# Performance work log

Hardware: AMD Instinct MI355X
Metric: run time of the kernel (lower is better)

Reference implementation:

```python
import jax, jax.numpy as jnp
import numpy as np

N, D, E, G, L = 65536, 512, 1048576, 128, 512


def setup_inputs() -> dict:
    key = jax.random.key(0)
    ks = jax.random.split(key, 12)
    s = 0.02
    # disjoint sequence groups: a permutation of all nodes reshaped to [G, L]
    seq_ids = jax.random.permutation(ks[0], N).reshape(G, L)
    return {
        'in_feats': jax.random.normal(ks[1], (N, D), jnp.float32),
        'edge_src': jax.random.randint(ks[2], (E,), 0, N),
        'edge_dst': jax.random.randint(ks[3], (E,), 0, N),
        'seq_ids': seq_ids,
        'W_conv': jax.random.normal(ks[4], (D, D), jnp.float32) * s,
        'b_conv': jnp.zeros((D,), jnp.float32),
        'W_ff1': jax.random.normal(ks[5], (D, D), jnp.float32) * s,
        'b_ff1': jnp.zeros((D,), jnp.float32),
        'W_ih': jax.random.normal(ks[6], (3 * D, D), jnp.float32) * s,
        'W_hh': jax.random.normal(ks[7], (3 * D, D), jnp.float32) * s,
        'b_ih': jnp.zeros((3 * D,), jnp.float32),
        'b_hh': jnp.zeros((3 * D,), jnp.float32),
        'W_ff2': jax.random.normal(ks[8], (D, D), jnp.float32) * s,
        'b_ff2': jnp.zeros((D,), jnp.float32),
    }


def _gru(x_lgd, W_ih, W_hh, b_ih, b_hh):
    # x_lgd: [L, G, D] (seq-major, batch_first=False); torch nn.GRU cell math
    d = W_hh.shape[1]
    # precompute input gates for all steps: [L, G, 3D]
    gi_all = jnp.einsum('lgd,ed->lge', x_lgd, W_ih) + b_ih

    def step(h, gi):
        gh = h @ W_hh.T + b_hh
        ir, iz, inn = jnp.split(gi, 3, axis=-1)
        hr, hz, hn = jnp.split(gh, 3, axis=-1)
        r = jax.nn.sigmoid(ir + hr)
        z = jax.nn.sigmoid(iz + hz)
        n = jnp.tanh(inn + r * hn)
        h_new = (1.0 - z) * n + z * h
        return h_new, h_new

    h0 = jnp.zeros((x_lgd.shape[1], d), x_lgd.dtype)
    _, ys = jax.lax.scan(step, h0, gi_all)
    return ys  # [L, G, D]


def reference(in_feats, edge_src, edge_dst, seq_ids, W_conv, b_conv,
              W_ff1, b_ff1, W_ih, W_hh, b_ih, b_hh, W_ff2, b_ff2):
    # conv_layer: mean aggregation over incoming edges, then Linear
    agg = jax.ops.segment_sum(in_feats[edge_src], edge_dst, num_segments=N)
    deg = jax.ops.segment_sum(jnp.ones((E,), in_feats.dtype), edge_dst, num_segments=N)
    agg = agg / jnp.maximum(deg, 1.0)[:, None]
    med = agg @ W_conv + b_conv                      # [N, D]
    # ff1
    med = jax.nn.relu(med @ W_ff1 + b_ff1)           # [N, D]
    # per-group seq_layer: gather [G, L, D], run GRU over L, scatter back
    seqs = med[seq_ids]                              # [G, L, D]
    ys = _gru(jnp.swapaxes(seqs, 0, 1), W_ih, W_hh, b_ih, b_hh)  # [L, G, D]
    ys = jnp.swapaxes(ys, 0, 1)                      # [G, L, D]
    # output[ids] += temp - output[ids]  ==  output[ids] = temp (disjoint ids)
    output = med.at[seq_ids.reshape(-1)].set(ys.reshape(-1, med.shape[-1]))
    # ff2
    return output @ W_ff2 + b_ff2
```

## Files before the change

kernel.cpp:

```cpp
#include <hip/hip_runtime.h>
#include <hip/hip_bf16.h>
#include <stdint.h>

typedef __hip_bfloat16 bf16;
typedef __attribute__((ext_vector_type(8))) short short8;
typedef __attribute__((ext_vector_type(4))) float f32x4;
typedef __attribute__((ext_vector_type(4))) unsigned int u32x4;
typedef __attribute__((ext_vector_type(2))) unsigned int u32x2;

#define NN 65536
#define DD 512
#define EE 1048576
#define GG 128
#define LL 512

static __device__ __forceinline__ void gld_lds16(const void* g, void* l) {
  __builtin_amdgcn_global_load_lds((const __attribute__((address_space(1))) uint32_t*)g,
                                   (__attribute__((address_space(3))) uint32_t*)l, 16, 0, 0);
}

__global__ __launch_bounds__(256) void k_prep(
    const float* __restrict__ Wc, const float* __restrict__ Wf1, const float* __restrict__ Wf2,
    const float* __restrict__ Wih, const float* __restrict__ Whh,
    bf16* __restrict__ WcT, bf16* __restrict__ Wf1T, bf16* __restrict__ Wf2T,
    bf16* __restrict__ WihB, bf16* __restrict__ WhhB)
{
  const int i = blockIdx.x * 256 + threadIdx.x;
  if (i < 512 * 512) {
    const int k = i >> 9, n = i & 511;
    WcT [n * 512 + k] = __float2bfloat16(Wc [i]);
    Wf1T[n * 512 + k] = __float2bfloat16(Wf1[i]);
    Wf2T[n * 512 + k] = __float2bfloat16(Wf2[i]);
  }
  if (i < 1536 * 512) {
    WihB[i] = __float2bfloat16(Wih[i]);
    WhhB[i] = __float2bfloat16(Whh[i]);
  }
}

__global__ __launch_bounds__(256) void k_cast(const float* __restrict__ f, bf16* __restrict__ o) {
  const long i = (long)(blockIdx.x * 256 + threadIdx.x) * 4;
  const float4 v = *(const float4*)&f[i];
  union { bf16 b[4]; ushort4 u; } pk;
  pk.b[0] = __float2bfloat16(v.x);
  pk.b[1] = __float2bfloat16(v.y);
  pk.b[2] = __float2bfloat16(v.z);
  pk.b[3] = __float2bfloat16(v.w);
  *(ushort4*)&o[i] = pk.u;
}

__global__ __launch_bounds__(256) void k_deg(const int* __restrict__ dst, int* __restrict__ deg) {
  const int e = blockIdx.x * 256 + threadIdx.x;
  atomicAdd(&deg[dst[e]], 1);
}

__global__ __launch_bounds__(1024) void k_scan1(const int* __restrict__ deg,
                                                int* __restrict__ roff, int* __restrict__ partial) {
  __shared__ int sd[1024];
  const int t = threadIdx.x, b = blockIdx.x, i = b * 1024 + t;
  const int v = deg[i];
  sd[t] = v;
  __syncthreads();
  for (int off = 1; off < 1024; off <<= 1) {
    int add = (t >= off) ? sd[t - off] : 0;
    __syncthreads();
    sd[t] += add;
    __syncthreads();
  }
  roff[i] = sd[t] - v;
  if (t == 1023) partial[b] = sd[t];
}

__global__ __launch_bounds__(64) void k_scan2(const int* __restrict__ partial, int* __restrict__ base) {
  __shared__ int sd[64];
  const int t = threadIdx.x;
  const int v = partial[t];
  sd[t] = v;
  __syncthreads();
  for (int off = 1; off < 64; off <<= 1) {
    int add = (t >= off) ? sd[t - off] : 0;
    __syncthreads();
    sd[t] += add;
    __syncthreads();
  }
  base[t] = sd[t] - v;
  if (t == 63) base[64] = sd[63];
}

__global__ __launch_bounds__(1024) void k_scan3(const int* __restrict__ base,
                                                int* __restrict__ roff, int* __restrict__ cursor) {
  const int b = blockIdx.x, t = threadIdx.x, i = b * 1024 + t;
  const int v = roff[i] + base[b];
  roff[i] = v;
  cursor[i] = v;
  if (i == 0) roff[NN] = base[64];
}

__global__ __launch_bounds__(256) void k_fill(const int* __restrict__ src, const int* __restrict__ dst,
                                              int* __restrict__ cursor, int* __restrict__ csr) {
  const int e = blockIdx.x * 256 + threadIdx.x;
  const int p = atomicAdd(&cursor[dst[e]], 1);
  csr[p] = src[e];
}

__global__ __launch_bounds__(128) void k_agg(
    const bf16* __restrict__ featsb, const int* __restrict__ csr,
    const int* __restrict__ roff, bf16* __restrict__ agg)
{
  const int n = blockIdx.x, t = threadIdx.x;
  const int s0 = roff[n], s1 = roff[n + 1];
  float a0 = 0.f, a1 = 0.f, a2 = 0.f, a3 = 0.f;
  for (int i = s0; i < s1; ++i) {
    const int s = csr[i];
    const ushort4 v = *(const ushort4*)&featsb[(long)s * 512 + t * 4];
    bf16 b0, b1, b2, b3;
    *(uint16_t*)&b0 = v.x; *(uint16_t*)&b1 = v.y;
    *(uint16_t*)&b2 = v.z; *(uint16_t*)&b3 = v.w;
    a0 += __bfloat162float(b0); a1 += __bfloat162float(b1);
    a2 += __bfloat162float(b2); a3 += __bfloat162float(b3);
  }
  const float sc = 1.f / fmaxf((float)(s1 - s0), 1.f);
  union { bf16 b[4]; ushort4 u; } pk;
  pk.b[0] = __float2bfloat16(a0 * sc);
  pk.b[1] = __float2bfloat16(a1 * sc);
  pk.b[2] = __float2bfloat16(a2 * sc);
  pk.b[3] = __float2bfloat16(a3 * sc);
  *(ushort4*)&agg[(long)n * 512 + t * 4] = pk.u;
}

template<bool GATHER, bool RELU>
__global__ __launch_bounds__(256) void k_gemm(
    const bf16* __restrict__ A, const bf16* __restrict__ Bt,
    const float* __restrict__ bias, const int* __restrict__ gidx,
    bf16* __restrict__ outb, int Ncols)
{
  __shared__ bf16 lsA[128 * 64];
  __shared__ bf16 lsB[128 * 64];
  const int t = threadIdx.x;
  const int lane = t & 63, wid = t >> 6;
  const int wr = wid >> 1, wc = wid & 1;
  const int tm = blockIdx.y * 128, tn = blockIdx.x * 128;
  const int col8 = (t & 7) * 8;
  const int rsub = t >> 3;
  const int lc = lane & 15, lk = lane >> 4;

  long arow[4], brow[4];
#pragma unroll
  for (int i = 0; i < 4; ++i) {
    const int r = tm + i * 32 + rsub;
    int ar = r;
    if constexpr (GATHER) ar = gidx[r];
    arow[i] = (long)ar * 512;
    brow[i] = (long)(tn + i * 32 + rsub) * 512;
  }

  f32x4 acc[4][4];
#pragma unroll
  for (int a = 0; a < 4; ++a)
#pragma unroll
    for (int b = 0; b < 4; ++b) acc[a][b] = (f32x4){0.f, 0.f, 0.f, 0.f};

  for (int ks = 0; ks < 8; ++ks) {
    const int k0 = ks * 64;
#pragma unroll
    for (int i = 0; i < 4; ++i) {
      gld_lds16(A  + arow[i] + k0 + col8, &lsA[i * 2048 + t * 8]);
      gld_lds16(Bt + brow[i] + k0 + col8, &lsB[i * 2048 + t * 8]);
    }
    __syncthreads();
#pragma unroll
    for (int kk = 0; kk < 2; ++kk) {
      short8 af[4], bfr[4];
#pragma unroll
      for (int mi = 0; mi < 4; ++mi)
        af[mi] = *(const short8*)&lsA[(wr * 64 + mi * 16 + lc) * 64 + kk * 32 + lk * 8];
#pragma unroll
      for (int ni = 0; ni < 4; ++ni)
        bfr[ni] = *(const short8*)&lsB[(wc * 64 + ni * 16 + lc) * 64 + kk * 32 + lk * 8];
#pragma unroll
      for (int mi = 0; mi < 4; ++mi)
#pragma unroll
        for (int ni = 0; ni < 4; ++ni)
          acc[mi][ni] = __builtin_amdgcn_mfma_f32_16x16x32_bf16(af[mi], bfr[ni], acc[mi][ni], 0, 0, 0);
    }
    __syncthreads();
  }

  float bv[4];
#pragma unroll
  for (int ni = 0; ni < 4; ++ni) bv[ni] = bias[tn + wc * 64 + ni * 16 + lc];

#pragma unroll
  for (int mi = 0; mi < 4; ++mi) {
    const int r0 = tm + wr * 64 + mi * 16 + lk * 4;
#pragma unroll
    for (int j = 0; j < 4; ++j) {
      const int row = r0 + j;
      const long orow = (long)row * Ncols;
#pragma unroll
      for (int ni = 0; ni < 4; ++ni) {
        float v = acc[mi][ni][j] + bv[ni];
        if constexpr (RELU) v = fmaxf(v, 0.f);
        const int c = tn + wc * 64 + ni * 16 + lc;
        outb[orow + c] = __float2bfloat16(v);
      }
    }
  }
}

__global__ __launch_bounds__(256) void k_gemm_ys(
    const uint8_t* __restrict__ Ay, const bf16* __restrict__ Bt,
    const float* __restrict__ bias, const int* __restrict__ gidx,
    float* __restrict__ outf)
{
  __shared__ bf16 lsA[128 * 64];
  __shared__ bf16 lsB[128 * 64];
  const int t = threadIdx.x;
  const int lane = t & 63, wid = t >> 6;
  const int wr = wid >> 1, wc = wid & 1;
  const int tm = blockIdx.y * 128, tn = blockIdx.x * 128;
  const int col8 = (t & 7) * 8;
  const int rsub = t >> 3;
  const int lc = lane & 15, lk = lane >> 4;

  long arow[4], brow[4];
#pragma unroll
  for (int i = 0; i < 4; ++i) {
    const int r = tm + i * 32 + rsub;
    const int g = r >> 9, l = r & 511;
    arow[i] = ((long)l * 8 + (g >> 4)) * 16384 + (g & 15) * 32;
    brow[i] = (long)(tn + i * 32 + rsub) * 512;
  }

  f32x4 acc[4][4];
#pragma unroll
  for (int a = 0; a < 4; ++a)
#pragma unroll
    for (int b = 0; b < 4; ++b) acc[a][b] = (f32x4){0.f, 0.f, 0.f, 0.f};

  for (int ks = 0; ks < 8; ++ks) {
    const int k0 = ks * 64;
    const int kk16 = k0 + col8;
    const long aoff = ((long)(kk16 >> 4) << 9) + ((kk16 & 15) << 1);
#pragma unroll
    for (int i = 0; i < 4; ++i) {
      gld_lds16(Ay + arow[i] + aoff, &lsA[i * 2048 + t * 8]);
      gld_lds16(Bt + brow[i] + k0 + col8, &lsB[i * 2048 + t * 8]);
    }
    __syncthreads();
#pragma unroll
    for (int kk = 0; kk < 2; ++kk) {
      short8 af[4], bfr[4];
#pragma unroll
      for (int mi = 0; mi < 4; ++mi)
        af[mi] = *(const short8*)&lsA[(wr * 64 + mi * 16 + lc) * 64 + kk * 32 + lk * 8];
#pragma unroll
      for (int ni = 0; ni < 4; ++ni)
        bfr[ni] = *(const short8*)&lsB[(wc * 64 + ni * 16 + lc) * 64 + kk * 32 + lk * 8];
#pragma unroll
      for (int mi = 0; mi < 4; ++mi)
#pragma unroll
        for (int ni = 0; ni < 4; ++ni)
          acc[mi][ni] = __builtin_amdgcn_mfma_f32_16x16x32_bf16(af[mi], bfr[ni], acc[mi][ni], 0, 0, 0);
    }
    __syncthreads();
  }

  float bv[4];
#pragma unroll
  for (int ni = 0; ni < 4; ++ni) bv[ni] = bias[tn + wc * 64 + ni * 16 + lc];

#pragma unroll
  for (int mi = 0; mi < 4; ++mi) {
    const int r0 = tm + wr * 64 + mi * 16 + lk * 4;
#pragma unroll
    for (int j = 0; j < 4; ++j) {
      const int row = r0 + j;
      const long orow = (long)gidx[row] * 512;
#pragma unroll
      for (int ni = 0; ni < 4; ++ni) {
        const int c = tn + wc * 64 + ni * 16 + lc;
        outf[orow + c] = acc[mi][ni][j] + bv[ni];
      }
    }
  }
}

__global__ __launch_bounds__(128, 1) void k_gru12(
    const bf16* __restrict__ Whh, const float* __restrict__ bhh,
    const bf16* __restrict__ gi, uint8_t* __restrict__ ys2, int* __restrict__ flags)
{
  __shared__ bf16 lsW[96 * 520];
  const int t = threadIdx.x, lane = t & 63, w = t >> 6;
  const int chain = blockIdx.x >> 4, jcb = blockIdx.x & 15;
  const int lc = lane & 15, lk = lane >> 4;
  const int g0 = chain * 16;
  const int cols0 = jcb * 32;
  const int p = jcb * 2 + w;
  const int d0 = p * 16 + lk * 4;

#pragma unroll
  for (int it = 0; it < 48; ++it) {
    const int c = it * 128 + t;
    const int row = c >> 6, col8 = (c & 63) * 8;
    const int e = ((row >> 5) << 9) + cols0 + (row & 31);
    *(uint4*)&lsW[row * 520 + col8] = *(const uint4*)&Whh[(long)e * 512 + col8];
  }
  __syncthreads();

  float bRa[4], bZa[4], bNa[4];
#pragma unroll
  for (int j = 0; j < 4; ++j) {
    bRa[j] = bhh[d0 + j];
    bZa[j] = bhh[512 + d0 + j];
    bNa[j] = bhh[1024 + d0 + j];
  }
  float hreg[4] = {0.f, 0.f, 0.f, 0.f};

  const bf16* gp = gi + (long)(g0 + lc) * 786432 + d0;
  uint8_t* psto = ys2 + (long)chain * 16384 + p * 512 + lc * 32 + lk * 8;
  const long laneoff = (long)(lk >> 1) * 512 + lc * 32 + (lk & 1) * 16;

  int* chflags = flags + chain * 32 * 32;
  int* myflag  = chflags + p * 32;

  for (int l = 0; l < 512; ++l) {
    u32x2 gRv, gZv, gNv;
    asm volatile("global_load_dwordx2 %0, %1, off"             : "=v"(gRv) : "v"(gp) : "memory");
    asm volatile("global_load_dwordx2 %0, %1, off offset:1024" : "=v"(gZv) : "v"(gp) : "memory");
    asm volatile("global_load_dwordx2 %0, %1, off offset:2048" : "=v"(gNv) : "v"(gp) : "memory");
    gp += 1536;

    f32x4 acc[3] = { (f32x4){0.f,0.f,0.f,0.f}, (f32x4){0.f,0.f,0.f,0.f}, (f32x4){0.f,0.f,0.f,0.f} };
    if (l > 0) {
      int ok;
      do {
        const int v = __hip_atomic_load(&chflags[(lane & 31) * 32], __ATOMIC_RELAXED,
                                        __HIP_MEMORY_SCOPE_AGENT);
        ok = __all(v >= l);
      } while (!ok);
      asm volatile("" ::: "memory");

      const uint8_t* pb = ys2 + ((long)(l - 1) * 8 + chain) * 16384 + laneoff;
      u32x4 hv[16];
#pragma unroll
      for (int q = 0; q < 4; ++q) {
        const uint8_t* pbq = pb + q * 4096;
#pragma unroll
        for (int r2 = 0; r2 < 4; ++r2)
          asm volatile("global_load_dwordx4 %0, %1, off offset:%2 sc0 sc1"
                       : "=v"(hv[q * 4 + r2]) : "v"(pbq), "n"(r2 * 1024) : "memory");
      }
      asm volatile("s_waitcnt vmcnt(0)" ::: "memory");
      __builtin_amdgcn_sched_barrier(0);

#pragma unroll
      for (int kk = 0; kk < 16; ++kk) {
        union { u32x4 u; short8 s; } cv;
        cv.u = hv[kk];
#pragma unroll
        for (int gate = 0; gate < 3; ++gate) {
          const short8 wfr = *(const short8*)&lsW[(gate * 32 + w * 16 + lc) * 520 + kk * 32 + lk * 8];
          acc[gate] = __builtin_amdgcn_mfma_f32_16x16x32_bf16(wfr, cv.s, acc[gate], 0, 0, 0);
        }
      }
    } else {
      asm volatile("s_waitcnt vmcnt(0)" ::: "memory");
      __builtin_amdgcn_sched_barrier(0);
    }

    uint32_t hb[4];
#pragma unroll
    for (int j = 0; j < 4; ++j) {
      const uint32_t sh = (j & 1) * 16;
      union { uint32_t u; float f; } cR, cZ, cN;
      cR.u = ((gRv[j >> 1] >> sh) & 0xffffu) << 16;
      cZ.u = ((gZv[j >> 1] >> sh) & 0xffffu) << 16;
      cN.u = ((gNv[j >> 1] >> sh) & 0xffffu) << 16;
      const float r = 1.f / (1.f + __expf(-(cR.f + acc[0][j] + bRa[j])));
      const float z = 1.f / (1.f + __expf(-(cZ.f + acc[1][j] + bZa[j])));
      const float x2 = cN.f + r * (acc[2][j] + bNa[j]);
      const float ex = __expf(2.f * x2);
      const float n = 1.f - 2.f / (ex + 1.f);
      const float hn = (1.f - z) * n + z * hreg[j];
      hreg[j] = hn;
      const bf16 hnb = __float2bfloat16(hn);
      hb[j] = (uint32_t)(*(const uint16_t*)&hnb);
    }
    u32x2 hp;
    hp[0] = hb[0] | (hb[1] << 16);
    hp[1] = hb[2] | (hb[3] << 16);
    asm volatile("global_store_dwordx2 %0, %1, off sc0 sc1" :: "v"(psto), "v"(hp) : "memory");
    psto += 131072;
    asm volatile("s_waitcnt vmcnt(0)" ::: "memory");
    if (lane == 0)
      __hip_atomic_store(myflag, l + 1, __ATOMIC_RELAXED, __HIP_MEMORY_SCOPE_AGENT);
  }
}

extern "C" void kernel_launch(void* const* d_in, const int* in_sizes, int n_in,
                              void* d_out, int out_size, void* d_ws, size_t ws_size,
                              hipStream_t stream)
{
  (void)in_sizes; (void)n_in; (void)out_size; (void)ws_size;
  const float* in_feats = (const float*)d_in[0];
  const int*   e_src    = (const int*)d_in[1];
  const int*   e_dst    = (const int*)d_in[2];
  const int*   seq      = (const int*)d_in[3];
  const float* W_conv   = (const float*)d_in[4];
  const float* b_conv   = (const float*)d_in[5];
  const float* W_ff1    = (const float*)d_in[6];
  const float* b_ff1    = (const float*)d_in[7];
  const float* W_ih     = (const float*)d_in[8];
  const float* W_hh     = (const float*)d_in[9];
  const float* b_ih     = (const float*)d_in[10];
  const float* b_hh     = (const float*)d_in[11];
  const float* W_ff2    = (const float*)d_in[12];
  const float* b_ff2    = (const float*)d_in[13];

  uint8_t* ws = (uint8_t*)d_ws;
  int*  deg     = (int*) (ws + 0);
  int*  cursor  = (int*) (ws + 262144u);
  int*  roff    = (int*) (ws + 524288u);
  bf16* WcT     = (bf16*)(ws + 1048576u);
  bf16* Wf1T    = (bf16*)(ws + 1572864u);
  bf16* Wf2T    = (bf16*)(ws + 2097152u);
  bf16* WihB    = (bf16*)(ws + 2621440u);
  bf16* WhhB    = (bf16*)(ws + 4194304u);
  int*  csr     = (int*) (ws + 6291456u);
  int*  flags   = (int*) (ws + 10485760u);
  int*  partial = (int*) (ws + 10616832u);
  int*  sbase   = (int*) (ws + 10620928u);
  bf16* med2    = (bf16*)(ws + 16777216u);
  uint8_t* ys2  = (uint8_t*)med2;
  bf16* gib     = (bf16*)(ws + 83886080u);
  bf16* aggb    = (bf16*)(ws + 83886080u);
  bf16* med1    = (bf16*)(ws + 150994944u);
  bf16* featsb  = (bf16*)(ws + 150994944u);

  hipMemsetAsync(deg,   0, NN * 4,          stream);
  hipMemsetAsync(flags, 0, 8 * 32 * 32 * 4, stream);

  k_prep <<<3072, 256, 0, stream>>>(W_conv, W_ff1, W_ff2, W_ih, W_hh, WcT, Wf1T, Wf2T, WihB, WhhB);
  k_cast <<<NN * DD / 1024, 256, 0, stream>>>(in_feats, featsb);
  k_deg  <<<EE / 256, 256, 0, stream>>>(e_dst, deg);
  k_scan1<<<64, 1024, 0, stream>>>(deg, roff, partial);
  k_scan2<<<1, 64, 0, stream>>>(partial, sbase);
  k_scan3<<<64, 1024, 0, stream>>>(sbase, roff, cursor);
  k_fill <<<EE / 256, 256, 0, stream>>>(e_src, e_dst, cursor, csr);
  k_agg  <<<NN, 128, 0, stream>>>(featsb, csr, roff, aggb);

  dim3 g512(4, 512), g1536(12, 512);
  k_gemm<false, false><<<g512,  256, 0, stream>>>(aggb, WcT,  b_conv, nullptr, med1, 512);
  k_gemm<false, true ><<<g512,  256, 0, stream>>>(med1, Wf1T, b_ff1,  nullptr, med2, 512);
  k_gemm<true,  false><<<g1536, 256, 0, stream>>>(med2, WihB, b_ih,   seq,     gib,  1536);

  k_gru12<<<128, 128, 0, stream>>>(WhhB, b_hh, gib, ys2, flags);

  k_gemm_ys<<<g512, 256, 0, stream>>>(ys2, Wf2T, b_ff2, seq, (float*)d_out);
}
```

Baseline: 2.430 ms.

## Use one wave per GRU block covering 32 columns; unroll edge aggregation by four

The GRU recurrence kernel now runs one 64-thread wave per block, and each wave computes two 16-column tiles. This halves the number of producer flags that every step must poll, from 32 to 16 per chain, which shortens the cross-block barrier latency on the serial critical path. In exchange, each wave does twice the MFMA and gate work per step, and the weight loading into LDS is done by fewer threads. Separately, the aggregation gather loop is unrolled by four with bit-shift bf16-to-float conversion, so more feature loads are in flight at once.

```diff
diff --git a/kernel.cpp b/kernel.cpp
--- a/kernel.cpp
+++ b/kernel.cpp
@@ -110,14 +110,29 @@
   const int n = blockIdx.x, t = threadIdx.x;
   const int s0 = roff[n], s1 = roff[n + 1];
   float a0 = 0.f, a1 = 0.f, a2 = 0.f, a3 = 0.f;
-  for (int i = s0; i < s1; ++i) {
+  int i = s0;
+  for (; i + 4 <= s1; i += 4) {
+    const int sA = csr[i], sB = csr[i + 1], sC = csr[i + 2], sD = csr[i + 3];
+    const ushort4 vA = *(const ushort4*)&featsb[(long)sA * 512 + t * 4];
+    const ushort4 vB = *(const ushort4*)&featsb[(long)sB * 512 + t * 4];
+    const ushort4 vC = *(const ushort4*)&featsb[(long)sC * 512 + t * 4];
+    const ushort4 vD = *(const ushort4*)&featsb[(long)sD * 512 + t * 4];
+    union { uint32_t u; float f; } c;
+    c.u = (uint32_t)vA.x << 16; a0 += c.f;  c.u = (uint32_t)vA.y << 16; a1 += c.f;
+    c.u = (uint32_t)vA.z << 16; a2 += c.f;  c.u = (uint32_t)vA.w << 16; a3 += c.f;
+    c.u = (uint32_t)vB.x << 16; a0 += c.f;  c.u = (uint32_t)vB.y << 16; a1 += c.f;
+    c.u = (uint32_t)vB.z << 16; a2 += c.f;  c.u = (uint32_t)vB.w << 16; a3 += c.f;
+    c.u = (uint32_t)vC.x << 16; a0 += c.f;  c.u = (uint32_t)vC.y << 16; a1 += c.f;
+    c.u = (uint32_t)vC.z << 16; a2 += c.f;  c.u = (uint32_t)vC.w << 16; a3 += c.f;
+    c.u = (uint32_t)vD.x << 16; a0 += c.f;  c.u = (uint32_t)vD.y << 16; a1 += c.f;
+    c.u = (uint32_t)vD.z << 16; a2 += c.f;  c.u = (uint32_t)vD.w << 16; a3 += c.f;
+  }
+  for (; i < s1; ++i) {
     const int s = csr[i];
     const ushort4 v = *(const ushort4*)&featsb[(long)s * 512 + t * 4];
-    bf16 b0, b1, b2, b3;
-    *(uint16_t*)&b0 = v.x; *(uint16_t*)&b1 = v.y;
-    *(uint16_t*)&b2 = v.z; *(uint16_t*)&b3 = v.w;
-    a0 += __bfloat162float(b0); a1 += __bfloat162float(b1);
-    a2 += __bfloat162float(b2); a3 += __bfloat162float(b3);
+    union { uint32_t u; float f; } c;
+    c.u = (uint32_t)v.x << 16; a0 += c.f;  c.u = (uint32_t)v.y << 16; a1 += c.f;
+    c.u = (uint32_t)v.z << 16; a2 += c.f;  c.u = (uint32_t)v.w << 16; a3 += c.f;
   }
   const float sc = 1.f / fmaxf((float)(s1 - s0), 1.f);
   union { bf16 b[4]; ushort4 u; } pk;
@@ -286,56 +301,59 @@
   }
 }
 
-__global__ __launch_bounds__(128, 1) void k_gru12(
+__global__ __launch_bounds__(64, 1) void k_gru13(
     const bf16* __restrict__ Whh, const float* __restrict__ bhh,
     const bf16* __restrict__ gi, uint8_t* __restrict__ ys2, int* __restrict__ flags)
 {
   __shared__ bf16 lsW[96 * 520];
-  const int t = threadIdx.x, lane = t & 63, w = t >> 6;
-  const int chain = blockIdx.x >> 4, jcb = blockIdx.x & 15;
+  const int t = threadIdx.x, lane = t & 63;
+  const int chain = blockIdx.x >> 4, p = blockIdx.x & 15;
   const int lc = lane & 15, lk = lane >> 4;
   const int g0 = chain * 16;
-  const int cols0 = jcb * 32;
-  const int p = jcb * 2 + w;
-  const int d0 = p * 16 + lk * 4;
-
-#pragma unroll
-  for (int it = 0; it < 48; ++it) {
-    const int c = it * 128 + t;
+  const int cols0 = p * 32;
+  const int d0a = cols0 + lk * 4;
+  const int d0b = cols0 + 16 + lk * 4;
+
+  for (int it = 0; it < 96; ++it) {
+    const int c = it * 64 + t;
     const int row = c >> 6, col8 = (c & 63) * 8;
     const int e = ((row >> 5) << 9) + cols0 + (row & 31);
     *(uint4*)&lsW[row * 520 + col8] = *(const uint4*)&Whh[(long)e * 512 + col8];
   }
   __syncthreads();
 
-  float bRa[4], bZa[4], bNa[4];
+  float bRa[4], bZa[4], bNa[4], bRb[4], bZb[4], bNb[4];
 #pragma unroll
   for (int j = 0; j < 4; ++j) {
-    bRa[j] = bhh[d0 + j];
-    bZa[j] = bhh[512 + d0 + j];
-    bNa[j] = bhh[1024 + d0 + j];
-  }
-  float hreg[4] = {0.f, 0.f, 0.f, 0.f};
-
-  const bf16* gp = gi + (long)(g0 + lc) * 786432 + d0;
-  uint8_t* psto = ys2 + (long)chain * 16384 + p * 512 + lc * 32 + lk * 8;
+    bRa[j] = bhh[d0a + j];  bZa[j] = bhh[512 + d0a + j];  bNa[j] = bhh[1024 + d0a + j];
+    bRb[j] = bhh[d0b + j];  bZb[j] = bhh[512 + d0b + j];  bNb[j] = bhh[1024 + d0b + j];
+  }
+  float hregA[4] = {0.f, 0.f, 0.f, 0.f};
+  float hregB[4] = {0.f, 0.f, 0.f, 0.f};
+
+  const bf16* gp = gi + (long)(g0 + lc) * 786432 + d0a;
+  uint8_t* psto = ys2 + (long)chain * 16384 + p * 1024 + lc * 32 + lk * 8;
   const long laneoff = (long)(lk >> 1) * 512 + lc * 32 + (lk & 1) * 16;
 
-  int* chflags = flags + chain * 32 * 32;
+  int* chflags = flags + chain * 16 * 32;
   int* myflag  = chflags + p * 32;
 
   for (int l = 0; l < 512; ++l) {
-    u32x2 gRv, gZv, gNv;
-    asm volatile("global_load_dwordx2 %0, %1, off"             : "=v"(gRv) : "v"(gp) : "memory");
-    asm volatile("global_load_dwordx2 %0, %1, off offset:1024" : "=v"(gZv) : "v"(gp) : "memory");
-    asm volatile("global_load_dwordx2 %0, %1, off offset:2048" : "=v"(gNv) : "v"(gp) : "memory");
+    u32x2 gRa, gZa, gNa, gRb, gZb, gNb;
+    asm volatile("global_load_dwordx2 %0, %1, off"             : "=v"(gRa) : "v"(gp) : "memory");
+    asm volatile("global_load_dwordx2 %0, %1, off offset:1024" : "=v"(gZa) : "v"(gp) : "memory");
+    asm volatile("global_load_dwordx2 %0, %1, off offset:2048" : "=v"(gNa) : "v"(gp) : "memory");
+    asm volatile("global_load_dwordx2 %0, %1, off offset:32"   : "=v"(gRb) : "v"(gp) : "memory");
+    asm volatile("global_load_dwordx2 %0, %1, off offset:1056" : "=v"(gZb) : "v"(gp) : "memory");
+    asm volatile("global_load_dwordx2 %0, %1, off offset:2080" : "=v"(gNb) : "v"(gp) : "memory");
     gp += 1536;
 
-    f32x4 acc[3] = { (f32x4){0.f,0.f,0.f,0.f}, (f32x4){0.f,0.f,0.f,0.f}, (f32x4){0.f,0.f,0.f,0.f} };
+    f32x4 accA[3] = { (f32x4){0.f,0.f,0.f,0.f}, (f32x4){0.f,0.f,0.f,0.f}, (f32x4){0.f,0.f,0.f,0.f} };
+    f32x4 accB[3] = { (f32x4){0.f,0.f,0.f,0.f}, (f32x4){0.f,0.f,0.f,0.f}, (f32x4){0.f,0.f,0.f,0.f} };
     if (l > 0) {
       int ok;
       do {
-        const int v = __hip_atomic_load(&chflags[(lane & 31) * 32], __ATOMIC_RELAXED,
+        const int v = __hip_atomic_load(&chflags[(lane & 15) * 32], __ATOMIC_RELAXED,
                                         __HIP_MEMORY_SCOPE_AGENT);
         ok = __all(v >= l);
       } while (!ok);
@@ -360,8 +378,10 @@
         cv.u = hv[kk];
 #pragma unroll
         for (int gate = 0; gate < 3; ++gate) {
-          const short8 wfr = *(const short8*)&lsW[(gate * 32 + w * 16 + lc) * 520 + kk * 32 + lk * 8];
-          acc[gate] = __builtin_amdgcn_mfma_f32_16x16x32_bf16(wfr, cv.s, acc[gate], 0, 0, 0);
+          const short8 wfA = *(const short8*)&lsW[(gate * 32 + lc) * 520 + kk * 32 + lk * 8];
+          const short8 wfB = *(const short8*)&lsW[(gate * 32 + 16 + lc) * 520 + kk * 32 + lk * 8];
+          accA[gate] = __builtin_amdgcn_mfma_f32_16x16x32_bf16(wfA, cv.s, accA[gate], 0, 0, 0);
+          accB[gate] = __builtin_amdgcn_mfma_f32_16x16x32_bf16(wfB, cv.s, accB[gate], 0, 0, 0);
         }
       }
     } else {
@@ -369,28 +389,46 @@
       __builtin_amdgcn_sched_barrier(0);
     }
 
-    uint32_t hb[4];
+    uint32_t hbA[4], hbB[4];
 #pragma unroll
     for (int j = 0; j < 4; ++j) {
       const uint32_t sh = (j & 1) * 16;
       union { uint32_t u; float f; } cR, cZ, cN;
-      cR.u = ((gRv[j >> 1] >> sh) & 0xffffu) << 16;
-      cZ.u = ((gZv[j >> 1] >> sh) & 0xffffu) << 16;
-      cN.u = ((gNv[j >> 1] >> sh) & 0xffffu) << 16;
-      const float r = 1.f / (1.f + __expf(-(cR.f + acc[0][j] + bRa[j])));
-      const float z = 1.f / (1.f + __expf(-(cZ.f + acc[1][j] + bZa[j])));
-      const float x2 = cN.f + r * (acc[2][j] + bNa[j]);
+      cR.u = ((gRa[j >> 1] >> sh) & 0xffffu) << 16;
+      cZ.u = ((gZa[j >> 1] >> sh) & 0xffffu) << 16;
+      cN.u = ((gNa[j >> 1] >> sh) & 0xffffu) << 16;
+      const float r = 1.f / (1.f + __expf(-(cR.f + accA[0][j] + bRa[j])));
+      const float z = 1.f / (1.f + __expf(-(cZ.f + accA[1][j] + bZa[j])));
+      const float x2 = cN.f + r * (accA[2][j] + bNa[j]);
       const float ex = __expf(2.f * x2);
       const float n = 1.f - 2.f / (ex + 1.f);
-      const float hn = (1.f - z) * n + z * hreg[j];
-      hreg[j] = hn;
+      const float hn = (1.f - z) * n + z * hregA[j];
+      hregA[j] = hn;
       const bf16 hnb = __float2bfloat16(hn);
-      hb[j] = (uint32_t)(*(const uint16_t*)&hnb);
-    }
-    u32x2 hp;
-    hp[0] = hb[0] | (hb[1] << 16);
-    hp[1] = hb[2] | (hb[3] << 16);
-    asm volatile("global_store_dwordx2 %0, %1, off sc0 sc1" :: "v"(psto), "v"(hp) : "memory");
+      hbA[j] = (uint32_t)(*(const uint16_t*)&hnb);
+    }
+#pragma unroll
+    for (int j = 0; j < 4; ++j) {
+      const uint32_t sh = (j & 1) * 16;
+      union { uint32_t u; float f; } cR, cZ, cN;
+      cR.u = ((gRb[j >> 1] >> sh) & 0xffffu) << 16;
+      cZ.u = ((gZb[j >> 1] >> sh) & 0xffffu) << 16;
+      cN.u = ((gNb[j >> 1] >> sh) & 0xffffu) << 16;
+      const float r = 1.f / (1.f + __expf(-(cR.f + accB[0][j] + bRb[j])));
+      const float z = 1.f / (1.f + __expf(-(cZ.f + accB[1][j] + bZb[j])));
+      const float x2 = cN.f + r * (accB[2][j] + bNb[j]);
+      const float ex = __expf(2.f * x2);
+      const float n = 1.f - 2.f / (ex + 1.f);
+      const float hn = (1.f - z) * n + z * hregB[j];
+      hregB[j] = hn;
+      const bf16 hnb = __float2bfloat16(hn);
+      hbB[j] = (uint32_t)(*(const uint16_t*)&hnb);
+    }
+    u32x2 hpA, hpB;
+    hpA[0] = hbA[0] | (hbA[1] << 16);  hpA[1] = hbA[2] | (hbA[3] << 16);
+    hpB[0] = hbB[0] | (hbB[1] << 16);  hpB[1] = hbB[2] | (hbB[3] << 16);
+    asm volatile("global_store_dwordx2 %0, %1, off sc0 sc1" :: "v"(psto),       "v"(hpA) : "memory");
+    asm volatile("global_store_dwordx2 %0, %1, off offset:512 sc0 sc1" :: "v"(psto), "v"(hpB) : "memory");
     psto += 131072;
     asm volatile("s_waitcnt vmcnt(0)" ::: "memory");
     if (lane == 0)
@@ -439,7 +477,7 @@
   bf16* featsb  = (bf16*)(ws + 150994944u);
 
   hipMemsetAsync(deg,   0, NN * 4,          stream);
-  hipMemsetAsync(flags, 0, 8 * 32 * 32 * 4, stream);
+  hipMemsetAsync(flags, 0, 8 * 16 * 32 * 4, stream);
 
   k_prep <<<3072, 256, 0, stream>>>(W_conv, W_ff1, W_ff2, W_ih, W_hh, WcT, Wf1T, Wf2T, WihB, WhhB);
   k_cast <<<NN * DD / 1024, 256, 0, stream>>>(in_feats, featsb);
@@ -455,7 +493,7 @@
   k_gemm<false, true ><<<g512,  256, 0, stream>>>(med1, Wf1T, b_ff1,  nullptr, med2, 512);
   k_gemm<true,  false><<<g1536, 256, 0, stream>>>(med2, WihB, b_ih,   seq,     gib,  1536);
 
-  k_gru12<<<128, 128, 0, stream>>>(WhhB, b_hh, gib, ys2, flags);
+  k_gru13<<<128, 64, 0, stream>>>(WhhB, b_hh, gib, ys2, flags);
 
   k_gemm_ys<<<g512, 256, 0, stream>>>(ys2, Wf2T, b_ff2, seq, (float*)d_out);
 }
```

New measurement: 2.767 ms. 13.9% more time.

## Interleave two GRU chains per block and unroll neighbor aggregation by four

Applied to the files above, without the earlier changes.

The GRU recurrence kernel now launches 64 blocks, and each block processes two independent 16-sequence chains (A and B) in alternation. While one chain waits on its cross-block flag synchronization, the other's phase can proceed, with each chain's W_hh slice in LDS shared by both. Phases within a block still run sequentially, so the latency hiding depends on chain B's peers making progress while chain A waits. Separately, the edge aggregation loop is unrolled by four with independent gathers, and bf16 is widened to float with a plain shift.

```diff
diff --git a/kernel.cpp b/kernel.cpp
--- a/kernel.cpp
+++ b/kernel.cpp
@@ -110,14 +110,29 @@
   const int n = blockIdx.x, t = threadIdx.x;
   const int s0 = roff[n], s1 = roff[n + 1];
   float a0 = 0.f, a1 = 0.f, a2 = 0.f, a3 = 0.f;
-  for (int i = s0; i < s1; ++i) {
+  int i = s0;
+  for (; i + 4 <= s1; i += 4) {
+    const int sA = csr[i], sB = csr[i + 1], sC = csr[i + 2], sD = csr[i + 3];
+    const ushort4 vA = *(const ushort4*)&featsb[(long)sA * 512 + t * 4];
+    const ushort4 vB = *(const ushort4*)&featsb[(long)sB * 512 + t * 4];
+    const ushort4 vC = *(const ushort4*)&featsb[(long)sC * 512 + t * 4];
+    const ushort4 vD = *(const ushort4*)&featsb[(long)sD * 512 + t * 4];
+    union { uint32_t u; float f; } c;
+    c.u = (uint32_t)vA.x << 16; a0 += c.f;  c.u = (uint32_t)vA.y << 16; a1 += c.f;
+    c.u = (uint32_t)vA.z << 16; a2 += c.f;  c.u = (uint32_t)vA.w << 16; a3 += c.f;
+    c.u = (uint32_t)vB.x << 16; a0 += c.f;  c.u = (uint32_t)vB.y << 16; a1 += c.f;
+    c.u = (uint32_t)vB.z << 16; a2 += c.f;  c.u = (uint32_t)vB.w << 16; a3 += c.f;
+    c.u = (uint32_t)vC.x << 16; a0 += c.f;  c.u = (uint32_t)vC.y << 16; a1 += c.f;
+    c.u = (uint32_t)vC.z << 16; a2 += c.f;  c.u = (uint32_t)vC.w << 16; a3 += c.f;
+    c.u = (uint32_t)vD.x << 16; a0 += c.f;  c.u = (uint32_t)vD.y << 16; a1 += c.f;
+    c.u = (uint32_t)vD.z << 16; a2 += c.f;  c.u = (uint32_t)vD.w << 16; a3 += c.f;
+  }
+  for (; i < s1; ++i) {
     const int s = csr[i];
     const ushort4 v = *(const ushort4*)&featsb[(long)s * 512 + t * 4];
-    bf16 b0, b1, b2, b3;
-    *(uint16_t*)&b0 = v.x; *(uint16_t*)&b1 = v.y;
-    *(uint16_t*)&b2 = v.z; *(uint16_t*)&b3 = v.w;
-    a0 += __bfloat162float(b0); a1 += __bfloat162float(b1);
-    a2 += __bfloat162float(b2); a3 += __bfloat162float(b3);
+    union { uint32_t u; float f; } c;
+    c.u = (uint32_t)v.x << 16; a0 += c.f;  c.u = (uint32_t)v.y << 16; a1 += c.f;
+    c.u = (uint32_t)v.z << 16; a2 += c.f;  c.u = (uint32_t)v.w << 16; a3 += c.f;
   }
   const float sc = 1.f / fmaxf((float)(s1 - s0), 1.f);
   union { bf16 b[4]; ushort4 u; } pk;
@@ -286,15 +301,82 @@
   }
 }
 
-__global__ __launch_bounds__(128, 1) void k_gru12(
+#define GRU_PHASE(CCH, CF, MF, GR, GZ, GN, HREG, PST)                                       \
+  {                                                                                          \
+    f32x4 acc[3] = { (f32x4){0.f,0.f,0.f,0.f}, (f32x4){0.f,0.f,0.f,0.f},                     \
+                     (f32x4){0.f,0.f,0.f,0.f} };                                             \
+    if (l > 0) {                                                                             \
+      int ok;                                                                                \
+      do {                                                                                   \
+        const int v = __hip_atomic_load(&(CF)[(lane & 31) * 32], __ATOMIC_RELAXED,           \
+                                        __HIP_MEMORY_SCOPE_AGENT);                           \
+        ok = __all(v >= l);                                                                  \
+      } while (!ok);                                                                         \
+      asm volatile("" ::: "memory");                                                         \
+      const uint8_t* pb = ys2 + ((long)(l - 1) * 8 + (CCH)) * 16384 + laneoff;               \
+      u32x4 hv[16];                                                                          \
+      _Pragma("unroll")                                                                      \
+      for (int q = 0; q < 4; ++q) {                                                          \
+        const uint8_t* pbq = pb + q * 4096;                                                  \
+        _Pragma("unroll")                                                                    \
+        for (int r2 = 0; r2 < 4; ++r2)                                                       \
+          asm volatile("global_load_dwordx4 %0, %1, off offset:%2 sc0 sc1"                   \
+                       : "=v"(hv[q * 4 + r2]) : "v"(pbq), "n"(r2 * 1024) : "memory");        \
+      }                                                                                      \
+      asm volatile("s_waitcnt vmcnt(0)" ::: "memory");                                       \
+      __builtin_amdgcn_sched_barrier(0);                                                     \
+      _Pragma("unroll")                                                                      \
+      for (int kk = 0; kk < 16; ++kk) {                                                      \
+        union { u32x4 u; short8 s; } cv;                                                     \
+        cv.u = hv[kk];                                                                       \
+        _Pragma("unroll")                                                                    \
+        for (int gate = 0; gate < 3; ++gate) {                                               \
+          const short8 wfr = *(const short8*)&lsW[(gate * 32 + w * 16 + lc) * 520            \
+                                                  + kk * 32 + lk * 8];                       \
+          acc[gate] = __builtin_amdgcn_mfma_f32_16x16x32_bf16(wfr, cv.s, acc[gate], 0, 0, 0);\
+        }                                                                                    \
+      }                                                                                      \
+    } else {                                                                                 \
+      asm volatile("s_waitcnt vmcnt(0)" ::: "memory");                                       \
+      __builtin_amdgcn_sched_barrier(0);                                                     \
+    }                                                                                        \
+    uint32_t hb[4];                                                                          \
+    _Pragma("unroll")                                                                        \
+    for (int j = 0; j < 4; ++j) {                                                            \
+      const uint32_t sh = (j & 1) * 16;                                                      \
+      union { uint32_t u; float f; } cR, cZ, cN;                                             \
+      cR.u = (((GR)[j >> 1] >> sh) & 0xffffu) << 16;                                         \
+      cZ.u = (((GZ)[j >> 1] >> sh) & 0xffffu) << 16;                                         \
+      cN.u = (((GN)[j >> 1] >> sh) & 0xffffu) << 16;                                         \
+      const float r = 1.f / (1.f + __expf(-(cR.f + acc[0][j] + bRa[j])));                    \
+      const float z = 1.f / (1.f + __expf(-(cZ.f + acc[1][j] + bZa[j])));                    \
+      const float x2 = cN.f + r * (acc[2][j] + bNa[j]);                                      \
+      const float ex = __expf(2.f * x2);                                                     \
+      const float n = 1.f - 2.f / (ex + 1.f);                                                \
+      const float hn = (1.f - z) * n + z * (HREG)[j];                                        \
+      (HREG)[j] = hn;                                                                        \
+      const bf16 hnb = __float2bfloat16(hn);                                                 \
+      hb[j] = (uint32_t)(*(const uint16_t*)&hnb);                                            \
+    }                                                                                        \
+    u32x2 hp;                                                                                \
+    hp[0] = hb[0] | (hb[1] << 16);                                                           \
+    hp[1] = hb[2] | (hb[3] << 16);                                                           \
+    asm volatile("global_store_dwordx2 %0, %1, off sc0 sc1"                                  \
+                 :: "v"((PST) + (long)l * 131072), "v"(hp) : "memory");                      \
+    asm volatile("s_waitcnt vmcnt(0)" ::: "memory");                                         \
+    if (lane == 0)                                                                           \
+      __hip_atomic_store(MF, l + 1, __ATOMIC_RELAXED, __HIP_MEMORY_SCOPE_AGENT);             \
+  }
+
+__global__ __launch_bounds__(128, 1) void k_gru15(
     const bf16* __restrict__ Whh, const float* __restrict__ bhh,
     const bf16* __restrict__ gi, uint8_t* __restrict__ ys2, int* __restrict__ flags)
 {
   __shared__ bf16 lsW[96 * 520];
   const int t = threadIdx.x, lane = t & 63, w = t >> 6;
-  const int chain = blockIdx.x >> 4, jcb = blockIdx.x & 15;
+  const int jcb = blockIdx.x & 15, cpair = blockIdx.x >> 4;
+  const int cA = cpair, cB = cpair + 4;
   const int lc = lane & 15, lk = lane >> 4;
-  const int g0 = chain * 16;
   const int cols0 = jcb * 32;
   const int p = jcb * 2 + w;
   const int d0 = p * 16 + lk * 4;
@@ -315,88 +397,36 @@
     bZa[j] = bhh[512 + d0 + j];
     bNa[j] = bhh[1024 + d0 + j];
   }
-  float hreg[4] = {0.f, 0.f, 0.f, 0.f};
-
-  const bf16* gp = gi + (long)(g0 + lc) * 786432 + d0;
-  uint8_t* psto = ys2 + (long)chain * 16384 + p * 512 + lc * 32 + lk * 8;
+  float hregA[4] = {0.f, 0.f, 0.f, 0.f};
+  float hregB[4] = {0.f, 0.f, 0.f, 0.f};
+
+  const bf16* gpA = gi + (long)(cA * 16 + lc) * 786432 + d0;
+  const bf16* gpB = gi + (long)(cB * 16 + lc) * 786432 + d0;
+  uint8_t* psA = ys2 + (long)cA * 16384 + p * 512 + lc * 32 + lk * 8;
+  uint8_t* psB = ys2 + (long)cB * 16384 + p * 512 + lc * 32 + lk * 8;
   const long laneoff = (long)(lk >> 1) * 512 + lc * 32 + (lk & 1) * 16;
 
-  int* chflags = flags + chain * 32 * 32;
-  int* myflag  = chflags + p * 32;
+  int* cfA = flags + cA * 32 * 32;
+  int* cfB = flags + cB * 32 * 32;
+  int* mfA = cfA + p * 32;
+  int* mfB = cfB + p * 32;
 
   for (int l = 0; l < 512; ++l) {
-    u32x2 gRv, gZv, gNv;
-    asm volatile("global_load_dwordx2 %0, %1, off"             : "=v"(gRv) : "v"(gp) : "memory");
-    asm volatile("global_load_dwordx2 %0, %1, off offset:1024" : "=v"(gZv) : "v"(gp) : "memory");
-    asm volatile("global_load_dwordx2 %0, %1, off offset:2048" : "=v"(gNv) : "v"(gp) : "memory");
-    gp += 1536;
-
-    f32x4 acc[3] = { (f32x4){0.f,0.f,0.f,0.f}, (f32x4){0.f,0.f,0.f,0.f}, (f32x4){0.f,0.f,0.f,0.f} };
-    if (l > 0) {
-      int ok;
-      do {
-        const int v = __hip_atomic_load(&chflags[(lane & 31) * 32], __ATOMIC_RELAXED,
-                                        __HIP_MEMORY_SCOPE_AGENT);
-        ok = __all(v >= l);
-      } while (!ok);
-      asm volatile("" ::: "memory");
-
-      const uint8_t* pb = ys2 + ((long)(l - 1) * 8 + chain) * 16384 + laneoff;
-      u32x4 hv[16];
-#pragma unroll
-      for (int q = 0; q < 4; ++q) {
-        const uint8_t* pbq = pb + q * 4096;
-#pragma unroll
-        for (int r2 = 0; r2 < 4; ++r2)
-          asm volatile("global_load_dwordx4 %0, %1, off offset:%2 sc0 sc1"
-                       : "=v"(hv[q * 4 + r2]) : "v"(pbq), "n"(r2 * 1024) : "memory");
-      }
-      asm volatile("s_waitcnt vmcnt(0)" ::: "memory");
-      __builtin_amdgcn_sched_barrier(0);
-
-#pragma unroll
-      for (int kk = 0; kk < 16; ++kk) {
-        union { u32x4 u; short8 s; } cv;
-        cv.u = hv[kk];
-#pragma unroll
-        for (int gate = 0; gate < 3; ++gate) {
-          const short8 wfr = *(const short8*)&lsW[(gate * 32 + w * 16 + lc) * 520 + kk * 32 + lk * 8];
-          acc[gate] = __builtin_amdgcn_mfma_f32_16x16x32_bf16(wfr, cv.s, acc[gate], 0, 0, 0);
-        }
-      }
-    } else {
-      asm volatile("s_waitcnt vmcnt(0)" ::: "memory");
-      __builtin_amdgcn_sched_barrier(0);
-    }
-
-    uint32_t hb[4];
-#pragma unroll
-    for (int j = 0; j < 4; ++j) {
-      const uint32_t sh = (j & 1) * 16;
-      union { uint32_t u; float f; } cR, cZ, cN;
-      cR.u = ((gRv[j >> 1] >> sh) & 0xffffu) << 16;
-      cZ.u = ((gZv[j >> 1] >> sh) & 0xffffu) << 16;
-      cN.u = ((gNv[j >> 1] >> sh) & 0xffffu) << 16;
-      const float r = 1.f / (1.f + __expf(-(cR.f + acc[0][j] + bRa[j])));
-      const float z = 1.f / (1.f + __expf(-(cZ.f + acc[1][j] + bZa[j])));
-      const float x2 = cN.f + r * (acc[2][j] + bNa[j]);
-      const float ex = __expf(2.f * x2);
-      const float n = 1.f - 2.f / (ex + 1.f);
-      const float hn = (1.f - z) * n + z * hreg[j];
-      hreg[j] = hn;
-      const bf16 hnb = __float2bfloat16(hn);
-      hb[j] = (uint32_t)(*(const uint16_t*)&hnb);
-    }
-    u32x2 hp;
-    hp[0] = hb[0] | (hb[1] << 16);
-    hp[1] = hb[2] | (hb[3] << 16);
-    asm volatile("global_store_dwordx2 %0, %1, off sc0 sc1" :: "v"(psto), "v"(hp) : "memory");
-    psto += 131072;
-    asm volatile("s_waitcnt vmcnt(0)" ::: "memory");
-    if (lane == 0)
-      __hip_atomic_store(myflag, l + 1, __ATOMIC_RELAXED, __HIP_MEMORY_SCOPE_AGENT);
-  }
-}
+    u32x2 gRa, gZa, gNa, gRb, gZb, gNb;
+    asm volatile("global_load_dwordx2 %0, %1, off"             : "=v"(gRa) : "v"(gpA) : "memory");
+    asm volatile("global_load_dwordx2 %0, %1, off offset:1024" : "=v"(gZa) : "v"(gpA) : "memory");
+    asm volatile("global_load_dwordx2 %0, %1, off offset:2048" : "=v"(gNa) : "v"(gpA) : "memory");
+    asm volatile("global_load_dwordx2 %0, %1, off"             : "=v"(gRb) : "v"(gpB) : "memory");
+    asm volatile("global_load_dwordx2 %0, %1, off offset:1024" : "=v"(gZb) : "v"(gpB) : "memory");
+    asm volatile("global_load_dwordx2 %0, %1, off offset:2048" : "=v"(gNb) : "v"(gpB) : "memory");
+    gpA += 1536;
+    gpB += 1536;
+
+    GRU_PHASE(cA, cfA, mfA, gRa, gZa, gNa, hregA, psA)
+    GRU_PHASE(cB, cfB, mfB, gRb, gZb, gNb, hregB, psB)
+  }
+}
+#undef GRU_PHASE
 
 extern "C" void kernel_launch(void* const* d_in, const int* in_sizes, int n_in,
                               void* d_out, int out_size, void* d_ws, size_t ws_size,
@@ -455,7 +485,7 @@
   k_gemm<false, true ><<<g512,  256, 0, stream>>>(med1, Wf1T, b_ff1,  nullptr, med2, 512);
   k_gemm<true,  false><<<g1536, 256, 0, stream>>>(med2, WihB, b_ih,   seq,     gib,  1536);
 
-  k_gru12<<<128, 128, 0, stream>>>(WhhB, b_hh, gib, ys2, flags);
+  k_gru15<<<64, 128, 0, stream>>>(WhhB, b_hh, gib, ys2, flags);
 
   k_gemm_ys<<<g512, 256, 0, stream>>>(ys2, Wf2T, b_ff2, seq, (float*)d_out);
 }
```

Measured after the change: 3.174 ms. 1.31x slower.
